# Kernel optimization log

Measured on AMD Instinct MI355X. Metric: run time of the kernel, lower is better.

The kernel has to match this reference:

```python
import jax, jax.numpy as jnp
import numpy as np

N = 500000  # nodes (groups of k edges)
K = 32      # edges per node == MLP input width
E = N * K
H = 256     # hidden size


def setup_inputs() -> dict:
    key = jax.random.key(0)
    ks = jax.random.split(key, 12)
    def lin(kw, fan_in, fan_out):
        # torch nn.Linear default init: U(-1/sqrt(fan_in), 1/sqrt(fan_in))
        bound = 1.0 / np.sqrt(fan_in)
        return jax.random.uniform(kw, (fan_in, fan_out), jnp.float32, -bound, bound)
    return {
        "x": jax.random.normal(ks[0], (N, 3), jnp.float32),
        "edge_index": jax.random.randint(ks[1], (2, E), 0, N, jnp.int32),
        "edge_attr": jax.random.normal(ks[2], (E, 1), jnp.float32),
        "W1": lin(ks[3], K, H), "b1": jnp.zeros((H,), jnp.float32),
        "W2": lin(ks[4], H, H), "b2": jnp.zeros((H,), jnp.float32),
        "W3": lin(ks[5], H, H), "b3": jnp.zeros((H,), jnp.float32),
        "W4": lin(ks[6], H, 1), "b4": jnp.zeros((1,), jnp.float32),
    }


def reference(x, edge_index, edge_attr, W1, b1, W2, b2, W3, b3, W4, b4):
    # message() returns edge_attr; aggregate() reshapes all messages to (-1, k)
    # (index is ignored), then runs the 4-layer MLP. x/edge_index unused in math.
    g = edge_attr.reshape(-1, K)                      # [N, K]
    h = jnp.tanh(g @ W1 + b1)                         # [N, H]
    h = jnp.tanh(h @ W2 + b2)                         # [N, H]
    h = jnp.tanh(h @ W3 + b3)                         # [N, H]
    out = jax.nn.log_sigmoid(h @ W4 + b4)             # [N, 1]
    return jnp.squeeze(out, 1)                        # [N]
```

## Files before the change

### kernel.cpp

```cpp
#include <hip/hip_runtime.h>
#include <stdint.h>

#define NN 500000
#define HH 256
#define NBLK ((NN + 63) / 64)
#define NCH 17

typedef short short8 __attribute__((ext_vector_type(8)));
typedef float floatx4 __attribute__((ext_vector_type(4)));

__device__ __forceinline__ unsigned short f2bf(float f) {
  union { float f; uint32_t u; } v; v.f = f;
  uint32_t r = v.u + 0x7fffu + ((v.u >> 16) & 1u);
  return (unsigned short)(r >> 16);
}
__device__ __forceinline__ float bf2f(unsigned short h) {
  union { uint32_t u; float f; } v; v.u = ((uint32_t)h) << 16;
  return v.f;
}
__device__ __forceinline__ float tanh_fast(float x) {
  float xc = fminf(fmaxf(x, -9.0f), 9.0f);
  float e = __expf(2.0f * xc);
  return __fdividef(e - 1.0f, e + 1.0f);
}
__device__ __forceinline__ float log_sigmoid_f(float x) {
  return fminf(x, 0.0f) - log1pf(__expf(-fabsf(x)));
}

__global__ void __launch_bounds__(256)
pack_weights(const float* __restrict__ W1, const float* __restrict__ W2,
             const float* __restrict__ W3, uint16_t* __restrict__ ws16) {
  int t = blockIdx.x * 256 + threadIdx.x;
  if (t >= NCH * 8192) return;
  int ch = t >> 13;
  int r = t & 8191;
  int n  = r & 255;
  int kp = r >> 8;
  float w;
  if (ch == 0)      w = W1[kp * HH + n];
  else if (ch <= 8) w = W2[((ch - 1) * 32 + kp) * HH + n];
  else              w = W3[((ch - 9) * 32 + kp) * HH + n];
  unsigned short hi = f2bf(w);
  unsigned short lo = f2bf(w - bf2f(hi));
  uint16_t* p = ws16 + (size_t)ch * 16384 + n * 32 + kp;
  p[0]    = hi;
  p[8192] = lo;
}

#define KSTEP_G(AHI, ALO, WG)                                                  \
  {                                                                            \
    const uint16_t* wg_ = (WG);                                                \
    _Pragma("unroll")                                                          \
    for (int nt = 0; nt < 4; ++nt) {                                           \
      short8 bhi = *(const short8*)(wg_ + woff + nt * 512);                    \
      short8 blo = *(const short8*)(wg_ + 8192 + woff + nt * 512);             \
      _Pragma("unroll")                                                        \
      for (int mt = 0; mt < 2; ++mt) {                                         \
        acc[mt][nt] = __builtin_amdgcn_mfma_f32_16x16x32_bf16(AHI[mt], bhi, acc[mt][nt], 0, 0, 0); \
        acc[mt][nt] = __builtin_amdgcn_mfma_f32_16x16x32_bf16(ALO[mt], bhi, acc[mt][nt], 0, 0, 0); \
        acc[mt][nt] = __builtin_amdgcn_mfma_f32_16x16x32_bf16(AHI[mt], blo, acc[mt][nt], 0, 0, 0); \
      }                                                                        \
    }                                                                          \
  }

#define ZEROACC()                                                              \
  {                                                                            \
    _Pragma("unroll") for (int mt = 0; mt < 2; ++mt)                           \
        _Pragma("unroll") for (int nt = 0; nt < 4; ++nt)                       \
            acc[mt][nt] = (floatx4){0.f, 0.f, 0.f, 0.f};                       \
  }

#define EPILOGUE_PACK(BIAS)                                                    \
  {                                                                            \
    _Pragma("unroll")                                                          \
    for (int nt = 0; nt < 4; ++nt) {                                           \
      float bv = (BIAS)[cb + nt * 16 + c];                                     \
      _Pragma("unroll")                                                        \
      for (int mt = 0; mt < 2; ++mt) {                                         \
        _Pragma("unroll")                                                      \
        for (int rr = 0; rr < 4; ++rr) {                                       \
          float tv = tanh_fast(acc[mt][nt][rr] + bv);                          \
          unsigned short h_ = f2bf(tv);                                        \
          unsigned short l_ = f2bf(tv - bf2f(h_));                             \
          int row = wr * 32 + mt * 16 + q * 4 + rr;                            \
          int k = cb + nt * 16 + c;                                            \
          hbuf[row * 256 + ((((k >> 2) ^ (row & 15)) << 2) | (k & 3))] =       \
              (uint32_t)h_ | ((uint32_t)l_ << 16);                             \
        }                                                                      \
      }                                                                        \
    }                                                                          \
  }

__global__ void __launch_bounds__(512, 4)
mlp_fused(const float* __restrict__ ea, const float* __restrict__ b1,
          const float* __restrict__ b2, const float* __restrict__ b3,
          const float* __restrict__ W4, const float* __restrict__ b4p,
          const uint16_t* __restrict__ wsw, float* __restrict__ out) {
  __shared__ uint32_t hbuf[16384];

  const int tid = threadIdx.x;
  const int wave = tid >> 6;
  const int lane = tid & 63;
  const int q = lane >> 4;
  const int c = lane & 15;
  const int wr = wave >> 2;
  const int wc = wave & 3;
  const int cb = wc * 64;
  const int blk = blockIdx.x;
  const int woff = (cb + c) * 32 + q * 8;

  floatx4 acc[2][4];

  short8 g_hi[2], g_lo[2];
#pragma unroll
  for (int mt = 0; mt < 2; ++mt) {
    int row = blk * 64 + wr * 32 + mt * 16 + c;
    if (row >= NN) row = NN - 1;
    const float* gp = ea + (size_t)row * 32 + q * 8;
    floatx4 v0 = *(const floatx4*)gp;
    floatx4 v1 = *(const floatx4*)(gp + 4);
    float g8[8] = {v0[0], v0[1], v0[2], v0[3], v1[0], v1[1], v1[2], v1[3]};
#pragma unroll
    for (int j = 0; j < 8; ++j) {
      unsigned short h_ = f2bf(g8[j]);
      g_hi[mt][j] = (short)h_;
      g_lo[mt][j] = (short)f2bf(g8[j] - bf2f(h_));
    }
  }

  ZEROACC();
  KSTEP_G(g_hi, g_lo, wsw);
  EPILOGUE_PACK(b1);
  __syncthreads();

#pragma unroll 1
  for (int lay = 0; lay < 2; ++lay) {
    ZEROACC();
#pragma unroll
    for (int kc = 0; kc < 8; ++kc) {
      const uint16_t* wg = wsw + (size_t)(1 + lay * 8 + kc) * 16384;
      short8 ahi[2], alo[2];
#pragma unroll
      for (int mt = 0; mt < 2; ++mt) {
        const int row = wr * 32 + mt * 16 + c;
        const uint32_t* hb = hbuf + row * 256;
        const int g0 = kc * 8 + q * 2;
        uint4 p0 = *(const uint4*)(hb + (((g0) ^ (row & 15)) << 2));
        uint4 p1 = *(const uint4*)(hb + (((g0 + 1) ^ (row & 15)) << 2));
        uint32_t u[8] = {p0.x, p0.y, p0.z, p0.w, p1.x, p1.y, p1.z, p1.w};
#pragma unroll
        for (int j = 0; j < 8; ++j) {
          ahi[mt][j] = (short)(u[j] & 0xffffu);
          alo[mt][j] = (short)(u[j] >> 16);
        }
      }
      KSTEP_G(ahi, alo, wg);
    }
    if (lay == 0) {
      __syncthreads();
      EPILOGUE_PACK(b2);
      __syncthreads();
    }
  }

  float p[2][4];
#pragma unroll
  for (int mt = 0; mt < 2; ++mt)
#pragma unroll
    for (int rr = 0; rr < 4; ++rr) p[mt][rr] = 0.0f;
#pragma unroll
  for (int nt = 0; nt < 4; ++nt) {
    float bv = b3[cb + nt * 16 + c];
    float wv = W4[cb + nt * 16 + c];
#pragma unroll
    for (int mt = 0; mt < 2; ++mt)
#pragma unroll
      for (int rr = 0; rr < 4; ++rr)
        p[mt][rr] += tanh_fast(acc[mt][nt][rr] + bv) * wv;
  }
#pragma unroll
  for (int off = 1; off < 16; off <<= 1)
#pragma unroll
    for (int mt = 0; mt < 2; ++mt)
#pragma unroll
      for (int rr = 0; rr < 4; ++rr)
        p[mt][rr] += __shfl_xor(p[mt][rr], off, 64);
  __syncthreads();
  float* red = (float*)hbuf;
  if (c == 0) {
#pragma unroll
    for (int mt = 0; mt < 2; ++mt)
#pragma unroll
      for (int rr = 0; rr < 4; ++rr)
        red[wc * 64 + wr * 32 + mt * 16 + q * 4 + rr] = p[mt][rr];
  }
  __syncthreads();
  if (tid < 64) {
    int row = blk * 64 + tid;
    float s = red[tid] + red[64 + tid] + red[128 + tid] + red[192 + tid] + b4p[0];
    if (row < NN) out[row] = log_sigmoid_f(s);
  }
}

extern "C" void kernel_launch(void* const* d_in, const int* in_sizes, int n_in,
                              void* d_out, int out_size, void* d_ws, size_t ws_size,
                              hipStream_t stream) {
  const float* ea = (const float*)d_in[2];
  const float* W1 = (const float*)d_in[3];
  const float* b1 = (const float*)d_in[4];
  const float* W2 = (const float*)d_in[5];
  const float* b2 = (const float*)d_in[6];
  const float* W3 = (const float*)d_in[7];
  const float* b3 = (const float*)d_in[8];
  const float* W4 = (const float*)d_in[9];
  const float* b4 = (const float*)d_in[10];

  pack_weights<<<(NCH * 8192 + 255) / 256, 256, 0, stream>>>(
      W1, W2, W3, (uint16_t*)d_ws);
  mlp_fused<<<NBLK, 512, 0, stream>>>(ea, b1, b2, b3, W4, b4,
                                      (const uint16_t*)d_ws, (float*)d_out);
}
```

Baseline: 764.1 us.

## Shrink block tile to 32 rows and store activations as split bf16 planes

Reduces the per-block row tile from 64 to 32 rows, with each of the 8 waves covering a 32-column slice of all rows. The hidden-state buffer becomes two separate bf16 planes (hi and lo) in a 32 KB shared array, so operand fragments load directly as short8 without unpacking. bf16 hi/lo splitting now truncates instead of rounding, and launch bounds ask for 8 blocks per CU. The intent is higher occupancy and cheaper LDS traffic, at the cost of twice as many weight loads per row. It also drops the tail guard, relying on N being divisible by 32.

```diff
diff --git a/kernel.cpp b/kernel.cpp
--- a/kernel.cpp
+++ b/kernel.cpp
@@ -3,19 +3,22 @@
 
 #define NN 500000
 #define HH 256
-#define NBLK ((NN + 63) / 64)
+#define MBLK 32
+#define NBLK (NN / MBLK)
 #define NCH 17
 
 typedef short short8 __attribute__((ext_vector_type(8)));
 typedef float floatx4 __attribute__((ext_vector_type(4)));
 
+union fu32 { float f; uint32_t u; };
+
 __device__ __forceinline__ unsigned short f2bf(float f) {
-  union { float f; uint32_t u; } v; v.f = f;
+  fu32 v; v.f = f;
   uint32_t r = v.u + 0x7fffu + ((v.u >> 16) & 1u);
   return (unsigned short)(r >> 16);
 }
 __device__ __forceinline__ float bf2f(unsigned short h) {
-  union { uint32_t u; float f; } v; v.u = ((uint32_t)h) << 16;
+  fu32 v; v.u = ((uint32_t)h) << 16;
   return v.f;
 }
 __device__ __forceinline__ float tanh_fast(float x) {
@@ -51,7 +54,7 @@
   {                                                                            \
     const uint16_t* wg_ = (WG);                                                \
     _Pragma("unroll")                                                          \
-    for (int nt = 0; nt < 4; ++nt) {                                           \
+    for (int nt = 0; nt < 2; ++nt) {                                           \
       short8 bhi = *(const short8*)(wg_ + woff + nt * 512);                    \
       short8 blo = *(const short8*)(wg_ + 8192 + woff + nt * 512);             \
       _Pragma("unroll")                                                        \
@@ -66,71 +69,72 @@
 #define ZEROACC()                                                              \
   {                                                                            \
     _Pragma("unroll") for (int mt = 0; mt < 2; ++mt)                           \
-        _Pragma("unroll") for (int nt = 0; nt < 4; ++nt)                       \
+        _Pragma("unroll") for (int nt = 0; nt < 2; ++nt)                       \
             acc[mt][nt] = (floatx4){0.f, 0.f, 0.f, 0.f};                       \
   }
 
-#define EPILOGUE_PACK(BIAS)                                                    \
+#define EPILOGUE_SPLIT(BIAS)                                                   \
   {                                                                            \
     _Pragma("unroll")                                                          \
-    for (int nt = 0; nt < 4; ++nt) {                                           \
-      float bv = (BIAS)[cb + nt * 16 + c];                                     \
+    for (int nt = 0; nt < 2; ++nt) {                                           \
+      const int k = wv * 32 + nt * 16 + c;                                     \
+      float bv = (BIAS)[k];                                                    \
       _Pragma("unroll")                                                        \
       for (int mt = 0; mt < 2; ++mt) {                                         \
         _Pragma("unroll")                                                      \
         for (int rr = 0; rr < 4; ++rr) {                                       \
           float tv = tanh_fast(acc[mt][nt][rr] + bv);                          \
-          unsigned short h_ = f2bf(tv);                                        \
-          unsigned short l_ = f2bf(tv - bf2f(h_));                             \
-          int row = wr * 32 + mt * 16 + q * 4 + rr;                            \
-          int k = cb + nt * 16 + c;                                            \
-          hbuf[row * 256 + ((((k >> 2) ^ (row & 15)) << 2) | (k & 3))] =       \
-              (uint32_t)h_ | ((uint32_t)l_ << 16);                             \
+          const int row = mt * 16 + q * 4 + rr;                                \
+          const int idx = row * 256 + ((((k >> 3) ^ (row & 15)) << 3) | (k & 7)); \
+          fu32 a_; a_.f = tv;                                                  \
+          hbuf[idx] = (uint16_t)(a_.u >> 16);                    \
+          fu32 h_; h_.u = a_.u & 0xffff0000u;                                  \
+          fu32 l_; l_.f = tv - h_.f;                                           \
+          hbuf[8192 + idx] = (uint16_t)(l_.u >> 16);             \
         }                                                                      \
       }                                                                        \
     }                                                                          \
   }
 
-__global__ void __launch_bounds__(512, 4)
+__global__ void __launch_bounds__(512, 8)
 mlp_fused(const float* __restrict__ ea, const float* __restrict__ b1,
           const float* __restrict__ b2, const float* __restrict__ b3,
           const float* __restrict__ W4, const float* __restrict__ b4p,
           const uint16_t* __restrict__ wsw, float* __restrict__ out) {
-  __shared__ uint32_t hbuf[16384];
+  __shared__ uint16_t hbuf[16384];
 
   const int tid = threadIdx.x;
-  const int wave = tid >> 6;
+  const int wv = tid >> 6;
   const int lane = tid & 63;
   const int q = lane >> 4;
   const int c = lane & 15;
-  const int wr = wave >> 2;
-  const int wc = wave & 3;
-  const int cb = wc * 64;
   const int blk = blockIdx.x;
-  const int woff = (cb + c) * 32 + q * 8;
-
-  floatx4 acc[2][4];
+  const int woff = (wv * 32 + c) * 32 + q * 8;
+  const int abase = c * 256;
+
+  floatx4 acc[2][2];
 
   short8 g_hi[2], g_lo[2];
 #pragma unroll
   for (int mt = 0; mt < 2; ++mt) {
-    int row = blk * 64 + wr * 32 + mt * 16 + c;
-    if (row >= NN) row = NN - 1;
+    int row = blk * 32 + mt * 16 + c;
     const float* gp = ea + (size_t)row * 32 + q * 8;
     floatx4 v0 = *(const floatx4*)gp;
     floatx4 v1 = *(const floatx4*)(gp + 4);
     float g8[8] = {v0[0], v0[1], v0[2], v0[3], v1[0], v1[1], v1[2], v1[3]};
 #pragma unroll
     for (int j = 0; j < 8; ++j) {
-      unsigned short h_ = f2bf(g8[j]);
-      g_hi[mt][j] = (short)h_;
-      g_lo[mt][j] = (short)f2bf(g8[j] - bf2f(h_));
+      fu32 a_; a_.f = g8[j];
+      g_hi[mt][j] = (short)(a_.u >> 16);
+      fu32 h_; h_.u = a_.u & 0xffff0000u;
+      fu32 l_; l_.f = g8[j] - h_.f;
+      g_lo[mt][j] = (short)(l_.u >> 16);
     }
   }
 
   ZEROACC();
   KSTEP_G(g_hi, g_lo, wsw);
-  EPILOGUE_PACK(b1);
+  EPILOGUE_SPLIT(b1);
   __syncthreads();
 
 #pragma unroll 1
@@ -142,23 +146,15 @@
       short8 ahi[2], alo[2];
 #pragma unroll
       for (int mt = 0; mt < 2; ++mt) {
-        const int row = wr * 32 + mt * 16 + c;
-        const uint32_t* hb = hbuf + row * 256;
-        const int g0 = kc * 8 + q * 2;
-        uint4 p0 = *(const uint4*)(hb + (((g0) ^ (row & 15)) << 2));
-        uint4 p1 = *(const uint4*)(hb + (((g0 + 1) ^ (row & 15)) << 2));
-        uint32_t u[8] = {p0.x, p0.y, p0.z, p0.w, p1.x, p1.y, p1.z, p1.w};
-#pragma unroll
-        for (int j = 0; j < 8; ++j) {
-          ahi[mt][j] = (short)(u[j] & 0xffffu);
-          alo[mt][j] = (short)(u[j] >> 16);
-        }
+        const int off = mt * 4096 + abase + (((kc * 4 + q) ^ c) << 3);
+        ahi[mt] = *(const short8*)(hbuf + off);
+        alo[mt] = *(const short8*)(hbuf + 8192 + off);
       }
       KSTEP_G(ahi, alo, wg);
     }
     if (lay == 0) {
       __syncthreads();
-      EPILOGUE_PACK(b2);
+      EPILOGUE_SPLIT(b2);
       __syncthreads();
     }
   }
@@ -169,14 +165,15 @@
 #pragma unroll
     for (int rr = 0; rr < 4; ++rr) p[mt][rr] = 0.0f;
 #pragma unroll
-  for (int nt = 0; nt < 4; ++nt) {
-    float bv = b3[cb + nt * 16 + c];
-    float wv = W4[cb + nt * 16 + c];
+  for (int nt = 0; nt < 2; ++nt) {
+    const int k = wv * 32 + nt * 16 + c;
+    float bv = b3[k];
+    float wv4 = W4[k];
 #pragma unroll
     for (int mt = 0; mt < 2; ++mt)
 #pragma unroll
       for (int rr = 0; rr < 4; ++rr)
-        p[mt][rr] += tanh_fast(acc[mt][nt][rr] + bv) * wv;
+        p[mt][rr] += tanh_fast(acc[mt][nt][rr] + bv) * wv4;
   }
 #pragma unroll
   for (int off = 1; off < 16; off <<= 1)
@@ -192,13 +189,14 @@
     for (int mt = 0; mt < 2; ++mt)
 #pragma unroll
       for (int rr = 0; rr < 4; ++rr)
-        red[wc * 64 + wr * 32 + mt * 16 + q * 4 + rr] = p[mt][rr];
+        red[wv * 32 + mt * 16 + q * 4 + rr] = p[mt][rr];
   }
   __syncthreads();
-  if (tid < 64) {
-    int row = blk * 64 + tid;
-    float s = red[tid] + red[64 + tid] + red[128 + tid] + red[192 + tid] + b4p[0];
-    if (row < NN) out[row] = log_sigmoid_f(s);
+  if (tid < 32) {
+    float s = b4p[0];
+#pragma unroll
+    for (int w = 0; w < 8; ++w) s += red[w * 32 + tid];
+    out[blk * 32 + tid] = log_sigmoid_f(s);
   }
 }
 
```

New measurement: 881.8 us. 15.4% more time.
